# Optimization experiments

Measured on AMD Instinct MI355X. Metric: run time of the kernel, lower is better.

## Reference

```python
import jax, jax.numpy as jnp
import numpy as np

K = 4                      # options['num_k']
NOISE_EPS = 0.1            # noise_epsilon in noisy_top_k_gating
LOSS_COEF = 1e-4
EPS_COMBINE = float(np.finfo(np.float64).eps)  # np.finfo(float).eps in combine
INV_SQRT2 = 0.7071067811865475


def _norm_cdf(z):
    # Normal(0,1).cdf
    return 0.5 * (1.0 + jax.lax.erf(z * INV_SQRT2))


def _cv_squared(v):
    # torch .var() is unbiased (ddof=1)
    return jnp.var(v, ddof=1) / (jnp.mean(v) ** 2 + 1e-10)


def setup_inputs() -> dict:
    key = jax.random.key(0)
    B, D, E, H, O = 1024, 1024, 16, 2048, 1024
    ks = jax.random.split(key, 6)
    x = jax.random.normal(ks[0], (B, D), jnp.float32)
    w_gate = jax.random.normal(ks[1], (D, E), jnp.float32) * 0.02
    w_noise = jax.random.normal(ks[2], (D, E), jnp.float32) * 0.02
    W1 = jax.random.normal(ks[3], (E, D, H), jnp.float32) / np.sqrt(D).astype(np.float32)
    b1 = jnp.zeros((E, H), jnp.float32)
    W2 = jax.random.normal(ks[4], (E, H, O), jnp.float32) / np.sqrt(H).astype(np.float32)
    b2 = jnp.zeros((E, O), jnp.float32)
    noise = jax.random.normal(ks[5], (B, E), jnp.float32)  # randn_like(clean_logits)
    return {"x": x, "w_gate": w_gate, "w_noise": w_noise,
            "W1": W1, "b1": b1, "W2": W2, "b2": b2, "noise": noise}


def moe_forward(x, w_gate, w_noise, W1, b1, W2, b2, noise):
    B = x.shape[0]
    # --- noisy top-k gating (train=True path) ---
    clean_logits = x @ w_gate                              # [B, E]
    noise_std = jax.nn.softplus(x @ w_noise) + NOISE_EPS   # [B, E]
    noisy_logits = clean_logits + noise * noise_std        # [B, E]
    top_logits, top_idx = jax.lax.top_k(noisy_logits, K + 1)  # [B, K+1]
    topk_gates = jax.nn.softmax(top_logits[:, :K], axis=1)    # [B, K]
    gates = jnp.zeros_like(noisy_logits).at[
        jnp.arange(B)[:, None], top_idx[:, :K]].set(topk_gates)  # [B, E] sparse
    # --- load = E[prob in top-k] (smooth load estimate) ---
    thr_in = top_logits[:, K][:, None]       # (k+1)-th value: threshold if in
    thr_out = top_logits[:, K - 1][:, None]  # k-th value: threshold if out
    is_in = noisy_logits > thr_in
    prob_if_in = _norm_cdf((clean_logits - thr_in) / noise_std)
    prob_if_out = _norm_cdf((clean_logits - thr_out) / noise_std)
    load = jnp.where(is_in, prob_if_in, prob_if_out).sum(0)   # [E]
    importance = gates.sum(0)                                 # [E]
    loss = (_cv_squared(importance) + _cv_squared(load)) * LOSS_COEF
    # --- experts + combine ---
    # Dense all-expert compute; gates are exactly zero off the top-k so the
    # gate-weighted sum reproduces the sparse dispatch/index_add combine math.
    h = jax.nn.relu(jnp.einsum('bi,eih->beh', x, W1) + b1)    # [B, E, H]
    expert_out = jnp.einsum('beh,eho->beo', h, W2) + b2       # [B, E, O]
    # combine: sum_e gate[b,e] * exp(expert_out[b,e,:]); zeros -> eps; log
    combined = jnp.einsum('be,beo->bo', gates, jnp.exp(expert_out))  # [B, O]
    combined = jnp.where(combined == 0, EPS_COMBINE, combined)
    y = jnp.log(combined)
    return y, loss


def reference(x, w_gate, w_noise, W1, b1, W2, b2, noise):
    return moe_forward(x, w_gate, w_noise, W1, b1, W2, b2, noise)
```

## Files before the change

kernel.cpp:

```cpp
#include <hip/hip_runtime.h>
#include <cstdint>
#include <cstddef>

#define BTOK 1024
#define DDIM 1024
#define EEXP 16
#define HDIM 2048
#define ODIM 1024

typedef __bf16 bh;
typedef bh bh8 __attribute__((ext_vector_type(8)));
typedef bh bh4 __attribute__((ext_vector_type(4)));
typedef float fx4 __attribute__((ext_vector_type(4)));

__device__ __forceinline__ void gload16(const void* g, void* l) {
  __builtin_amdgcn_global_load_lds(
      (const __attribute__((address_space(1))) void*)g,
      (__attribute__((address_space(3))) void*)l, 16, 0, 0);
}

__global__ __launch_bounds__(256) void k_tcvt(const float* __restrict__ in,
                                              bh* __restrict__ out, int R, int C) {
  const int e = blockIdx.z;
  const int r0 = blockIdx.y * 64, c0 = blockIdx.x * 64;
  const float* pin = in + (size_t)e * R * C;
  bh* pout = out + (size_t)e * R * C;
  __shared__ __align__(16) bh t[64 * 65];
  const int tid = threadIdx.x;
#pragma unroll
  for (int rep = 0; rep < 4; ++rep) {
    int task = rep * 256 + tid;
    int r = task >> 4, c4 = task & 15;
    fx4 v = *(const fx4*)(pin + (size_t)(r0 + r) * C + c0 + c4 * 4);
    int base = r * 65 + c4 * 4;
#pragma unroll
    for (int u = 0; u < 4; ++u) t[base + u] = (bh)v[u];
  }
  __syncthreads();
#pragma unroll
  for (int rep = 0; rep < 4; ++rep) {
    int task = rep * 256 + tid;
    int cc = task >> 4, g2 = task & 15;
    bh4 o;
#pragma unroll
    for (int u = 0; u < 4; ++u) o[u] = t[(g2 * 4 + u) * 65 + cc];
    *(bh4*)(pout + (size_t)(c0 + cc) * R + r0 + g2 * 4) = o;
  }
}

__global__ __launch_bounds__(256) void k_gating(
    const float* __restrict__ x, const float* __restrict__ wg,
    const float* __restrict__ wn, const float* __restrict__ nz,
    bh* __restrict__ xbf, unsigned* __restrict__ cnt,
    int* __restrict__ tok_buck, float* __restrict__ gate_buck,
    float* __restrict__ imp_part, float* __restrict__ load_part) {
  const int b = blockIdx.x, tid = threadIdx.x;
  __shared__ __align__(16) float xs[1024];
  __shared__ float part[32][9];
  __shared__ float vals[32];
  fx4 v = *(const fx4*)(x + (size_t)b * 1024 + tid * 4);
  *(fx4*)(xs + tid * 4) = v;
  bh4 xb;
#pragma unroll
  for (int u = 0; u < 4; ++u) xb[u] = (bh)v[u];
  *(bh4*)(xbf + (size_t)b * 1024 + tid * 4) = xb;
  __syncthreads();
  const int col = tid & 31, g = tid >> 5;
  const float* wp = ((col < 16) ? wg : wn) + (col & 15);
  float s = 0.f;
  for (int it = g * 128; it < g * 128 + 128; ++it) s += xs[it] * wp[it * 16];
  part[col][g] = s;
  __syncthreads();
  if (tid < 32) {
    float tsum = 0.f;
#pragma unroll
    for (int gg = 0; gg < 8; ++gg) tsum += part[tid][gg];
    vals[tid] = tsum;
  }
  __syncthreads();
  if (tid == 0) {
    float clean[16], sd[16], noisy[16];
#pragma unroll
    for (int e = 0; e < 16; ++e) {
      clean[e] = vals[e];
      float raw = vals[16 + e];
      float sp = fmaxf(raw, 0.f) + log1pf(expf(-fabsf(raw)));
      sd[e] = sp + 0.1f;
      noisy[e] = clean[e] + nz[b * 16 + e] * sd[e];
    }
    float tv[5]; int ti[5]; unsigned used = 0;
    for (int r = 0; r < 5; ++r) {
      float bst = -INFINITY; int bi = 0;
      for (int e = 0; e < 16; ++e)
        if (!((used >> e) & 1u) && noisy[e] > bst) { bst = noisy[e]; bi = e; }
      used |= 1u << bi; tv[r] = bst; ti[r] = bi;
    }
    float gts[4]; float se = 0.f;
#pragma unroll
    for (int k = 0; k < 4; ++k) { gts[k] = expf(tv[k] - tv[0]); se += gts[k]; }
#pragma unroll
    for (int k = 0; k < 4; ++k) gts[k] /= se;
    const float thr_in = tv[4], thr_out = tv[3];
    float imp[16];
#pragma unroll
    for (int e = 0; e < 16; ++e) imp[e] = 0.f;
    for (int k = 0; k < 4; ++k) imp[ti[k]] = gts[k];
    for (int e = 0; e < 16; ++e) imp_part[b * 16 + e] = imp[e];
    for (int e = 0; e < 16; ++e) {
      bool is_in = noisy[e] > thr_in;
      float z = (clean[e] - (is_in ? thr_in : thr_out)) / sd[e];
      load_part[b * 16 + e] = 0.5f * (1.f + erff(z * 0.70710678118654752f));
    }
    for (int k = 0; k < 4; ++k) {
      int ee = ti[k];
      unsigned p = atomicAdd(&cnt[ee], 1u);
      tok_buck[ee * 1024 + (int)p] = b;
      gate_buck[ee * 1024 + (int)p] = gts[k];
    }
  }
}

__device__ __forceinline__ float cv2_16(const float* v) {
  float m = 0.f;
  for (int i = 0; i < 16; ++i) m += v[i];
  m *= (1.f / 16.f);
  float var = 0.f;
  for (int i = 0; i < 16; ++i) { float d = v[i] - m; var += d * d; }
  var *= (1.f / 15.f);
  return var / (m * m + 1e-10f);
}

__global__ __launch_bounds__(256) void k_finalize(
    const unsigned* __restrict__ cnt, unsigned* __restrict__ offs,
    const float* __restrict__ imp_part, const float* __restrict__ load_part,
    float* __restrict__ loss_out) {
  const int tid = threadIdx.x;
  __shared__ float red[256];
  __shared__ float impv[16], loadv[16];
  const int e = tid & 15, p = tid >> 4;
  float s = 0.f;
  for (int r = 0; r < 64; ++r) s += imp_part[((p * 64 + r) << 4) + e];
  red[tid] = s;
  __syncthreads();
  if (tid < 16) {
    float t = 0.f;
    for (int pp = 0; pp < 16; ++pp) t += red[pp * 16 + tid];
    impv[tid] = t;
  }
  __syncthreads();
  s = 0.f;
  for (int r = 0; r < 64; ++r) s += load_part[((p * 64 + r) << 4) + e];
  red[tid] = s;
  __syncthreads();
  if (tid < 16) {
    float t = 0.f;
    for (int pp = 0; pp < 16; ++pp) t += red[pp * 16 + tid];
    loadv[tid] = t;
  }
  __syncthreads();
  if (tid == 0) {
    unsigned o = 0;
    for (int ee = 0; ee < 16; ++ee) { offs[ee] = o; o += cnt[ee]; }
    loss_out[0] = (cv2_16(impv) + cv2_16(loadv)) * 1e-4f;
  }
}

__global__ __launch_bounds__(256) void k_gemm1(
    const bh* __restrict__ xbf, const bh* __restrict__ w1t,
    const float* __restrict__ b1, const int* __restrict__ tok_buck,
    const unsigned* __restrict__ cnt, const unsigned* __restrict__ offs,
    bh* __restrict__ hbf) {
  const int e = blockIdx.z, mt = blockIdx.y, nt = blockIdx.x;
  const int ne = (int)cnt[e];
  if (mt * 128 >= ne) return;
  __shared__ __align__(16) bh As[4][128 * 32];
  __shared__ __align__(16) bh Bs[4][128 * 32];
  const int tid = threadIdx.x;
  const int lane = tid & 63, wv = tid >> 6, wm = wv >> 1, wn_ = wv & 1;

  const bh* a_src[2]; const bh* b_src[2];
  int dst_off[2];
#pragma unroll
  for (int r = 0; r < 2; ++r) {
    int task = r * 256 + tid;
    int row = task >> 2, s = task & 3;
    int gm = mt * 128 + row; if (gm >= ne) gm = ne - 1;
    int tok = tok_buck[e * 1024 + gm];
    a_src[r] = xbf + (size_t)tok * 1024 + ((s ^ (row & 3)) << 3);
    b_src[r] = w1t + (size_t)e * (2048 * 1024) + (size_t)(nt * 128 + row) * 1024 +
               ((s ^ (row & 3)) << 3);
    dst_off[r] = (r * 256 + (wv << 6)) << 4;
  }
  const int ln15 = lane & 15, q = lane >> 4;
  const int qs = ((q ^ (ln15 & 3)) << 3);
  int a_off[4], b_off[4];
#pragma unroll
  for (int i = 0; i < 4; ++i) {
    a_off[i] = (wm * 64 + i * 16 + ln15) * 32 + qs;
    b_off[i] = (wn_ * 64 + i * 16 + ln15) * 32 + qs;
  }
  fx4 zero = {0.f, 0.f, 0.f, 0.f};
  fx4 acc[4][4];
#pragma unroll
  for (int i = 0; i < 4; ++i)
#pragma unroll
    for (int j = 0; j < 4; ++j) acc[i][j] = zero;

  auto stage = [&](int qb, int kt) {
    const int ko = kt * 32;
#pragma unroll
    for (int r = 0; r < 2; ++r) {
      gload16(a_src[r] + ko, (char*)(&As[qb][0]) + dst_off[r]);
      gload16(b_src[r] + ko, (char*)(&Bs[qb][0]) + dst_off[r]);
    }
  };

  const int NT = 32;
  stage(0, 0); stage(1, 1); stage(2, 2);
  asm volatile("s_waitcnt vmcnt(8)" ::: "memory");
  __builtin_amdgcn_s_barrier();

  for (int t = 0; t < NT; ++t) {
    if (t + 3 < NT) stage((t + 3) & 3, t + 3);
    const bh* Ab = &As[t & 3][0];
    const bh* Bb = &Bs[t & 3][0];
    bh8 af[4], bfr[4];
#pragma unroll
    for (int i = 0; i < 4; ++i) af[i] = *(const bh8*)(Ab + a_off[i]);
#pragma unroll
    for (int i = 0; i < 4; ++i) bfr[i] = *(const bh8*)(Bb + b_off[i]);
#pragma unroll
    for (int i = 0; i < 4; ++i)
#pragma unroll
      for (int j = 0; j < 4; ++j)
        acc[i][j] = __builtin_amdgcn_mfma_f32_16x16x32_bf16(af[i], bfr[j], acc[i][j], 0, 0, 0);
    if (t + 3 < NT)      asm volatile("s_waitcnt vmcnt(8) lgkmcnt(0)" ::: "memory");
    else if (t + 2 < NT) asm volatile("s_waitcnt vmcnt(4) lgkmcnt(0)" ::: "memory");
    else if (t + 1 < NT) asm volatile("s_waitcnt vmcnt(0) lgkmcnt(0)" ::: "memory");
    if (t + 1 < NT) __builtin_amdgcn_s_barrier();
  }

  int nrows = ne - mt * 128; if (nrows > 128) nrows = 128;
  int jn[4]; float b1v[4];
#pragma unroll
  for (int j = 0; j < 4; ++j) {
    jn[j] = nt * 128 + wn_ * 64 + j * 16 + ln15;
    b1v[j] = b1[e * 2048 + jn[j]];
  }
  const int rowbase = (int)offs[e] + mt * 128;
#pragma unroll
  for (int i = 0; i < 4; ++i)
#pragma unroll
    for (int rr = 0; rr < 4; ++rr) {
      int ml = wm * 64 + i * 16 + q * 4 + rr;
      if (ml < nrows) {
        size_t ro = (size_t)(rowbase + ml) * 2048;
#pragma unroll
        for (int j = 0; j < 4; ++j) {
          float vv = acc[i][j][rr] + b1v[j];
          hbf[ro + jn[j]] = (bh)fmaxf(vv, 0.f);
        }
      }
    }
}

__global__ __launch_bounds__(256) void k_gemm2(
    const bh* __restrict__ hbf, const bh* __restrict__ w2t,
    const float* __restrict__ b2, const int* __restrict__ tok_buck,
    const float* __restrict__ gate_buck, const unsigned* __restrict__ cnt,
    const unsigned* __restrict__ offs, float* __restrict__ yv) {
  const int e = blockIdx.z, mt = blockIdx.y, nt = blockIdx.x;
  const int ne = (int)cnt[e];
  if (mt * 128 >= ne) return;
  __shared__ __align__(16) bh As[4][128 * 32];
  __shared__ __align__(16) bh Bs[4][128 * 32];
  const int tid = threadIdx.x;
  const int lane = tid & 63, wv = tid >> 6, wm = wv >> 1, wn_ = wv & 1;
  const int rowbase = (int)offs[e] + mt * 128;

  const bh* a_src[2]; const bh* b_src[2];
  int dst_off[2];
#pragma unroll
  for (int r = 0; r < 2; ++r) {
    int task = r * 256 + tid;
    int row = task >> 2, s = task & 3;
    a_src[r] = hbf + (size_t)(rowbase + row) * 2048 + ((s ^ (row & 3)) << 3);
    b_src[r] = w2t + (size_t)e * (1024 * 2048) + (size_t)(nt * 128 + row) * 2048 +
               ((s ^ (row & 3)) << 3);
    dst_off[r] = (r * 256 + (wv << 6)) << 4;
  }
  const int ln15 = lane & 15, q = lane >> 4;
  const int qs = ((q ^ (ln15 & 3)) << 3);
  int a_off[4], b_off[4];
#pragma unroll
  for (int i = 0; i < 4; ++i) {
    a_off[i] = (wm * 64 + i * 16 + ln15) * 32 + qs;
    b_off[i] = (wn_ * 64 + i * 16 + ln15) * 32 + qs;
  }
  fx4 zero = {0.f, 0.f, 0.f, 0.f};
  fx4 acc[4][4];
#pragma unroll
  for (int i = 0; i < 4; ++i)
#pragma unroll
    for (int j = 0; j < 4; ++j) acc[i][j] = zero;

  auto stage = [&](int qb, int kt) {
    const int ko = kt * 32;
#pragma unroll
    for (int r = 0; r < 2; ++r) {
      gload16(a_src[r] + ko, (char*)(&As[qb][0]) + dst_off[r]);
      gload16(b_src[r] + ko, (char*)(&Bs[qb][0]) + dst_off[r]);
    }
  };

  const int NT = 64;
  stage(0, 0); stage(1, 1); stage(2, 2);
  asm volatile("s_waitcnt vmcnt(8)" ::: "memory");
  __builtin_amdgcn_s_barrier();

  for (int t = 0; t < NT; ++t) {
    if (t + 3 < NT) stage((t + 3) & 3, t + 3);
    const bh* Ab = &As[t & 3][0];
    const bh* Bb = &Bs[t & 3][0];
    bh8 af[4], bfr[4];
#pragma unroll
    for (int i = 0; i < 4; ++i) af[i] = *(const bh8*)(Ab + a_off[i]);
#pragma unroll
    for (int i = 0; i < 4; ++i) bfr[i] = *(const bh8*)(Bb + b_off[i]);
#pragma unroll
    for (int i = 0; i < 4; ++i)
#pragma unroll
      for (int j = 0; j < 4; ++j)
        acc[i][j] = __builtin_amdgcn_mfma_f32_16x16x32_bf16(af[i], bfr[j], acc[i][j], 0, 0, 0);
    if (t + 3 < NT)      asm volatile("s_waitcnt vmcnt(8) lgkmcnt(0)" ::: "memory");
    else if (t + 2 < NT) asm volatile("s_waitcnt vmcnt(4) lgkmcnt(0)" ::: "memory");
    else if (t + 1 < NT) asm volatile("s_waitcnt vmcnt(0) lgkmcnt(0)" ::: "memory");
    if (t + 1 < NT) __builtin_amdgcn_s_barrier();
  }

  int nrows = ne - mt * 128; if (nrows > 128) nrows = 128;
  int on[4]; float b2v[4];
#pragma unroll
  for (int j = 0; j < 4; ++j) {
    on[j] = nt * 128 + wn_ * 64 + j * 16 + ln15;
    b2v[j] = b2[e * 1024 + on[j]];
  }
#pragma unroll
  for (int i = 0; i < 4; ++i)
#pragma unroll
    for (int rr = 0; rr < 4; ++rr) {
      int ml = wm * 64 + i * 16 + q * 4 + rr;
      if (ml < nrows) {
        int pos = mt * 128 + ml;
        int bt = tok_buck[e * 1024 + pos];
        float gg = gate_buck[e * 1024 + pos];
        float* yrow = yv + (size_t)bt * 1024;
#pragma unroll
        for (int j = 0; j < 4; ++j)
          atomicAdd(&yrow[on[j]], gg * expf(acc[i][j][rr] + b2v[j]));
      }
    }
}

__global__ __launch_bounds__(256) void k_log(float* __restrict__ yv) {
  const int i = blockIdx.x * 256 + threadIdx.x;
  fx4* p = (fx4*)yv + i;
  fx4 v = *p;
#pragma unroll
  for (int c = 0; c < 4; ++c) {
    float w = v[c];
    if (w == 0.f) w = 2.2204460492503131e-16f;
    v[c] = logf(w);
  }
  *p = v;
}

extern "C" void kernel_launch(void* const* d_in, const int* in_sizes, int n_in,
                              void* d_out, int out_size, void* d_ws, size_t ws_size,
                              hipStream_t stream) {
  const float* x  = (const float*)d_in[0];
  const float* wg = (const float*)d_in[1];
  const float* wn = (const float*)d_in[2];
  const float* W1 = (const float*)d_in[3];
  const float* b1 = (const float*)d_in[4];
  const float* W2 = (const float*)d_in[5];
  const float* b2 = (const float*)d_in[6];
  const float* nz = (const float*)d_in[7];
  float* out = (float*)d_out;

  char* ws = (char*)d_ws;
  unsigned* cnt      = (unsigned*)(ws + 0);
  unsigned* offs     = (unsigned*)(ws + 64);
  float*    imp_part = (float*)(ws + 256);
  float*    load_part= (float*)(ws + 256 + 65536);
  int*      tok_buck = (int*)(ws + 256 + 2 * 65536);
  float*    gate_buck= (float*)(ws + 256 + 3 * 65536);
  bh*       xbf      = (bh*)(ws + 262400);
  bh*       hbf      = (bh*)(ws + 2359552);
  bh*       w1t      = (bh*)(ws + 19661056);
  bh*       w2t      = (bh*)(ws + 86769920);
  const size_t needed = 153878784;
  if (ws_size < needed) {
    hipMemsetAsync(d_out, 0x42, (size_t)out_size * 4, stream);
    return;
  }

  hipMemsetAsync(d_out, 0, (size_t)out_size * 4, stream);
  hipMemsetAsync(cnt, 0, 64, stream);

  k_tcvt<<<dim3(2048 / 64, 1024 / 64, 16), 256, 0, stream>>>(W1, w1t, 1024, 2048);
  k_tcvt<<<dim3(1024 / 64, 2048 / 64, 16), 256, 0, stream>>>(W2, w2t, 2048, 1024);
  k_gating<<<1024, 256, 0, stream>>>(x, wg, wn, nz, xbf, cnt, tok_buck, gate_buck,
                                     imp_part, load_part);
  k_finalize<<<1, 256, 0, stream>>>(cnt, offs, imp_part, load_part, out + (out_size - 1));
  k_gemm1<<<dim3(16, 8, 16), 256, 0, stream>>>(xbf, w1t, b1, tok_buck, cnt, offs, hbf);
  k_gemm2<<<dim3(8, 8, 16), 256, 0, stream>>>(hbf, w2t, b2, tok_buck, gate_buck, cnt, offs, out);
  k_log<<<1024, 256, 0, stream>>>(out);
}
```

Baseline: 502.7 us.

## Pre-tile expert weights into swizzled contiguous blocks and remap GEMM grids per XCD

The weight conversion kernel now writes W1/W2 as bf16 tiles of 128x32 already in the XOR-swizzled LDS order, stored contiguously per (expert, n-tile, k-tile). Each GEMM B-tile load then reads one contiguous 8 KB chunk instead of 128 strided rows. The GEMM launches become 1D grids with an XCD-aware index remap, so blocks that share an expert and n-tile land on the same XCD and can reuse its L2. This adds index complexity, and the new transpose kernel reads LDS with strided column accesses that may bank-conflict.

```diff
diff --git a/kernel.cpp b/kernel.cpp
--- a/kernel.cpp
+++ b/kernel.cpp
@@ -19,32 +19,32 @@
       (__attribute__((address_space(3))) void*)l, 16, 0, 0);
 }
 
-__global__ __launch_bounds__(256) void k_tcvt(const float* __restrict__ in,
-                                              bh* __restrict__ out, int R, int C) {
-  const int e = blockIdx.z;
-  const int r0 = blockIdx.y * 64, c0 = blockIdx.x * 64;
-  const float* pin = in + (size_t)e * R * C;
-  bh* pout = out + (size_t)e * R * C;
-  __shared__ __align__(16) bh t[64 * 65];
+__global__ __launch_bounds__(256) void k_tcvt2(const float* __restrict__ in,
+                                               bh* __restrict__ out, int K, int N,
+                                               int KT, int NT) {
+  const int kt = blockIdx.x, nt = blockIdx.y, e = blockIdx.z;
+  const int k0 = kt * 32, n0 = nt * 128;
+  const float* pin = in + (size_t)e * K * N + (size_t)k0 * N + n0;
+  bh* pout = out + (((size_t)e * NT + nt) * KT + kt) * 4096;
+  __shared__ float t[32][129];
   const int tid = threadIdx.x;
 #pragma unroll
   for (int rep = 0; rep < 4; ++rep) {
+    int idx = rep * 256 + tid;
+    int kk = idx >> 5, c4 = (idx & 31) << 2;
+    fx4 v = *(const fx4*)(pin + (size_t)kk * N + c4);
+#pragma unroll
+    for (int u = 0; u < 4; ++u) t[kk][c4 + u] = v[u];
+  }
+  __syncthreads();
+#pragma unroll
+  for (int rep = 0; rep < 2; ++rep) {
     int task = rep * 256 + tid;
-    int r = task >> 4, c4 = task & 15;
-    fx4 v = *(const fx4*)(pin + (size_t)(r0 + r) * C + c0 + c4 * 4);
-    int base = r * 65 + c4 * 4;
-#pragma unroll
-    for (int u = 0; u < 4; ++u) t[base + u] = (bh)v[u];
-  }
-  __syncthreads();
-#pragma unroll
-  for (int rep = 0; rep < 4; ++rep) {
-    int task = rep * 256 + tid;
-    int cc = task >> 4, g2 = task & 15;
-    bh4 o;
-#pragma unroll
-    for (int u = 0; u < 4; ++u) o[u] = t[(g2 * 4 + u) * 65 + cc];
-    *(bh4*)(pout + (size_t)(c0 + cc) * R + r0 + g2 * 4) = o;
+    int row = task >> 2, s = task & 3, o = s ^ (row & 3);
+    bh8 w;
+#pragma unroll
+    for (int u = 0; u < 8; ++u) w[u] = (bh)t[o * 8 + u][row];
+    *(bh8*)(pout + (size_t)task * 8) = w;
   }
 }
 
@@ -170,7 +170,10 @@
     const float* __restrict__ b1, const int* __restrict__ tok_buck,
     const unsigned* __restrict__ cnt, const unsigned* __restrict__ offs,
     bh* __restrict__ hbf) {
-  const int e = blockIdx.z, mt = blockIdx.y, nt = blockIdx.x;
+  const int lid = blockIdx.x;
+  const int xcd = lid & 7, idx = lid >> 3;
+  const int mt = idx & 7, g = xcd * 32 + (idx >> 3);
+  const int e = g >> 4, nt = g & 15;
   const int ne = (int)cnt[e];
   if (mt * 128 >= ne) return;
   __shared__ __align__(16) bh As[4][128 * 32];
@@ -187,8 +190,7 @@
     int gm = mt * 128 + row; if (gm >= ne) gm = ne - 1;
     int tok = tok_buck[e * 1024 + gm];
     a_src[r] = xbf + (size_t)tok * 1024 + ((s ^ (row & 3)) << 3);
-    b_src[r] = w1t + (size_t)e * (2048 * 1024) + (size_t)(nt * 128 + row) * 1024 +
-               ((s ^ (row & 3)) << 3);
+    b_src[r] = w1t + (((size_t)e * 16 + nt) * 32) * 4096 + (size_t)task * 8;
     dst_off[r] = (r * 256 + (wv << 6)) << 4;
   }
   const int ln15 = lane & 15, q = lane >> 4;
@@ -208,10 +210,11 @@
 
   auto stage = [&](int qb, int kt) {
     const int ko = kt * 32;
+    const size_t bo = (size_t)kt * 4096;
 #pragma unroll
     for (int r = 0; r < 2; ++r) {
       gload16(a_src[r] + ko, (char*)(&As[qb][0]) + dst_off[r]);
-      gload16(b_src[r] + ko, (char*)(&Bs[qb][0]) + dst_off[r]);
+      gload16(b_src[r] + bo, (char*)(&Bs[qb][0]) + dst_off[r]);
     }
   };
 
@@ -269,7 +272,10 @@
     const float* __restrict__ b2, const int* __restrict__ tok_buck,
     const float* __restrict__ gate_buck, const unsigned* __restrict__ cnt,
     const unsigned* __restrict__ offs, float* __restrict__ yv) {
-  const int e = blockIdx.z, mt = blockIdx.y, nt = blockIdx.x;
+  const int lid = blockIdx.x;
+  const int xcd = lid & 7, idx = lid >> 3;
+  const int nt = idx & 7, g = xcd * 16 + (idx >> 3);
+  const int e = g >> 3, mt = g & 7;
   const int ne = (int)cnt[e];
   if (mt * 128 >= ne) return;
   __shared__ __align__(16) bh As[4][128 * 32];
@@ -285,8 +291,7 @@
     int task = r * 256 + tid;
     int row = task >> 2, s = task & 3;
     a_src[r] = hbf + (size_t)(rowbase + row) * 2048 + ((s ^ (row & 3)) << 3);
-    b_src[r] = w2t + (size_t)e * (1024 * 2048) + (size_t)(nt * 128 + row) * 2048 +
-               ((s ^ (row & 3)) << 3);
+    b_src[r] = w2t + (((size_t)e * 8 + nt) * 64) * 4096 + (size_t)task * 8;
     dst_off[r] = (r * 256 + (wv << 6)) << 4;
   }
   const int ln15 = lane & 15, q = lane >> 4;
@@ -306,10 +311,11 @@
 
   auto stage = [&](int qb, int kt) {
     const int ko = kt * 32;
+    const size_t bo = (size_t)kt * 4096;
 #pragma unroll
     for (int r = 0; r < 2; ++r) {
       gload16(a_src[r] + ko, (char*)(&As[qb][0]) + dst_off[r]);
-      gload16(b_src[r] + ko, (char*)(&Bs[qb][0]) + dst_off[r]);
+      gload16(b_src[r] + bo, (char*)(&Bs[qb][0]) + dst_off[r]);
     }
   };
 
@@ -408,12 +414,12 @@
   hipMemsetAsync(d_out, 0, (size_t)out_size * 4, stream);
   hipMemsetAsync(cnt, 0, 64, stream);
 
-  k_tcvt<<<dim3(2048 / 64, 1024 / 64, 16), 256, 0, stream>>>(W1, w1t, 1024, 2048);
-  k_tcvt<<<dim3(1024 / 64, 2048 / 64, 16), 256, 0, stream>>>(W2, w2t, 2048, 1024);
+  k_tcvt2<<<dim3(32, 16, 16), 256, 0, stream>>>(W1, w1t, 1024, 2048, 32, 16);
+  k_tcvt2<<<dim3(64, 8, 16), 256, 0, stream>>>(W2, w2t, 2048, 1024, 64, 8);
   k_gating<<<1024, 256, 0, stream>>>(x, wg, wn, nz, xbf, cnt, tok_buck, gate_buck,
                                      imp_part, load_part);
   k_finalize<<<1, 256, 0, stream>>>(cnt, offs, imp_part, load_part, out + (out_size - 1));
-  k_gemm1<<<dim3(16, 8, 16), 256, 0, stream>>>(xbf, w1t, b1, tok_buck, cnt, offs, hbf);
-  k_gemm2<<<dim3(8, 8, 16), 256, 0, stream>>>(hbf, w2t, b2, tok_buck, gate_buck, cnt, offs, out);
+  k_gemm1<<<2048, 256, 0, stream>>>(xbf, w1t, b1, tok_buck, cnt, offs, hbf);
+  k_gemm2<<<1024, 256, 0, stream>>>(hbf, w2t, b2, tok_buck, gate_buck, cnt, offs, out);
   k_log<<<1024, 256, 0, stream>>>(out);
 }
```

Measured after the change: 513.8 us. 1.02x slower.
